# Kernel tuning notes

Hardware: AMD Instinct MI355X
Metric: run time of the kernel (lower is better)

## Reference

```python
import jax, jax.numpy as jnp
from jax import lax
import numpy as np

NPOINT = 1024
RADII = (0.1, 0.2, 0.4)
NSAMPLES = (16, 32, 64)
MLPS = ((64, 64, 128), (128, 128, 256), (128, 128, 256))
IN_CH = 64  # 3 (xyz) + 61 (point features)
EPS = 1e-5


def setup_inputs() -> dict:
    key = jax.random.key(0)
    ks = jax.random.split(key, 64)
    inp = {
        "xyz": jax.random.normal(ks[0], (8, 3, 16384), dtype=jnp.float32),
        "points": jax.random.normal(ks[1], (8, 61, 16384), dtype=jnp.float32),
    }
    ki = 2
    for i, mlp in enumerate(MLPS):
        last = IN_CH
        for j, out_ch in enumerate(mlp):
            inp[f"w{i}{j}"] = jax.random.normal(ks[ki], (out_ch, last), dtype=jnp.float32) * 0.05
            inp[f"b{i}{j}"] = jnp.zeros((out_ch,), dtype=jnp.float32)
            inp[f"g{i}{j}"] = jnp.ones((out_ch,), dtype=jnp.float32)
            inp[f"bt{i}{j}"] = jnp.zeros((out_ch,), dtype=jnp.float32)
            last = out_ch
            ki += 1
    return inp


def square_distance(src, dst):
    # src [B,S,3], dst [B,N,3] -> [B,S,N]
    d = -2.0 * jnp.einsum("bsc,bnc->bsn", src, dst)
    d = d + jnp.sum(src * src, -1)[:, :, None]
    d = d + jnp.sum(dst * dst, -1)[:, None, :]
    return d


def farthest_point_sample(xyz, npoint):
    # xyz [B,N,3] -> idx [B,npoint]; deterministic start at index 0
    B, N, _ = xyz.shape
    def step(carry, _):
        distance, farthest = carry
        centroid = jnp.take_along_axis(xyz, farthest[:, None, None], axis=1)  # [B,1,3]
        dist = jnp.sum((xyz - centroid) ** 2, axis=-1)  # [B,N]
        distance = jnp.minimum(distance, dist)
        return (distance, jnp.argmax(distance, axis=-1).astype(jnp.int32)), farthest
    init = (jnp.full((B, N), 1e10, dtype=xyz.dtype), jnp.zeros((B,), dtype=jnp.int32))
    _, idxs = lax.scan(step, init, None, length=npoint)
    return idxs.T  # [B,npoint]


def gather_points(p, idx):
    # p [B,N,C], idx [B,...] -> [B,...,C]
    B = p.shape[0]
    flat = idx.reshape(B, -1)
    g = jnp.take_along_axis(p, flat[:, :, None], axis=1)
    return g.reshape(idx.shape + (p.shape[-1],))


def query_ball_points(radius, nsample, xyz, new_xyz):
    # xyz [B,N,3], new_xyz [B,S,3] -> idx [B,S,nsample]
    B, N, _ = xyz.shape
    d = square_distance(new_xyz, xyz)  # [B,S,N]
    idx = jnp.broadcast_to(jnp.arange(N, dtype=jnp.int32), d.shape)
    idx = jnp.where(d > radius * radius, N, idx)
    idx = jnp.sort(idx, axis=-1)[:, :, :nsample]
    first = idx[:, :, :1]
    return jnp.where(idx == N, first, idx)


def _forward(xyz, points, params):
    xyz_t = jnp.transpose(xyz, (0, 2, 1))       # [B,N,3]
    pts_t = jnp.transpose(points, (0, 2, 1))    # [B,N,D]
    B, N, _ = xyz_t.shape
    fps_idx = farthest_point_sample(xyz_t, NPOINT)
    new_xyz = gather_points(xyz_t, fps_idx)     # [B,S,3]
    feats = []
    for i, (radius, K) in enumerate(zip(RADII, NSAMPLES)):
        gidx = query_ball_points(radius, K, xyz_t, new_xyz)      # [B,S,K]
        grouped_xyz = gather_points(xyz_t, gidx) - new_xyz[:, :, None, :]
        grouped_pts = gather_points(pts_t, gidx)
        x = jnp.concatenate([grouped_xyz, grouped_pts], axis=-1)  # [B,S,K,IN_CH]
        for (w, b, g, bt) in params[i]:
            x = jnp.einsum("bskc,oc->bsko", x, w) + b  # 1x1 conv
            mean = jnp.mean(x, axis=(0, 1, 2))
            var = jnp.var(x, axis=(0, 1, 2))
            x = jax.nn.relu(g * (x - mean) * lax.rsqrt(var + EPS) + bt)
        feats.append(jnp.max(x, axis=2))  # [B,S,Cout]
    new_points = jnp.transpose(jnp.concatenate(feats, axis=-1), (0, 2, 1))  # [B,640,S]
    return jnp.transpose(new_xyz, (0, 2, 1)), new_points


def reference(xyz, points,
              w00, b00, g00, bt00, w01, b01, g01, bt01, w02, b02, g02, bt02,
              w10, b10, g10, bt10, w11, b11, g11, bt11, w12, b12, g12, bt12,
              w20, b20, g20, bt20, w21, b21, g21, bt21, w22, b22, g22, bt22):
    params = [
        [(w00, b00, g00, bt00), (w01, b01, g01, bt01), (w02, b02, g02, bt02)],
        [(w10, b10, g10, bt10), (w11, b11, g11, bt11), (w12, b12, g12, bt12)],
        [(w20, b20, g20, bt20), (w21, b21, g21, bt21), (w22, b22, g22, bt22)],
    ]
    return _forward(xyz, points, params)
```

## Files before the change

### kernel.cpp

```cpp
#include <hip/hip_runtime.h>
#include <stdint.h>

#define BB 8
#define NN 16384
#define SS 1024

typedef unsigned short u16;
typedef float f32x4 __attribute__((ext_vector_type(4)));
typedef short short8v __attribute__((ext_vector_type(8)));
typedef unsigned short us4 __attribute__((ext_vector_type(4)));
typedef unsigned short us8 __attribute__((ext_vector_type(8)));

static __device__ __forceinline__ float bf2f(u16 u){
    union { uint32_t u; float f; } v; v.u = ((uint32_t)u) << 16; return v.f;
}
static __device__ __forceinline__ u16 f2bf(float f){
    union { float f; uint32_t u; } v; v.f = f;
    return (u16)((v.u + 0x7FFFu + ((v.u >> 16) & 1u)) >> 16);
}
static constexpr int cmax2(int a, int b){ return a > b ? a : b; }

#define LP 12288

__global__ __launch_bounds__(1024) void fps_kernel(const float* __restrict__ xyz,
                                                   float* __restrict__ q,
                                                   float* __restrict__ out_xyz){
#pragma clang fp contract(off)
    __shared__ float lx[LP], ly[LP], lz[LP];
    __shared__ int hist[SS];
    __shared__ unsigned long long slot;
    int b = blockIdx.x;
    int t = threadIdx.x;
    const float* xb = xyz + (size_t)b*3*NN;
    float px[16], py[16], pz[16], dd[16];
#pragma unroll
    for (int j=0;j<16;++j){
        int n = t + j*1024;
        px[j] = xb[n];
        py[j] = xb[NN+n];
        pz[j] = xb[2*NN+n];
        dd[j] = 1e10f;
    }
    for (int idx = t; idx < LP; idx += 1024){
        lx[idx] = xb[idx];
        ly[idx] = xb[NN+idx];
        lz[idx] = xb[2*NN+idx];
    }
    if (t == 0) slot = 0ull;
    __syncthreads();

    int lane = t & 63;
    int far = 0;
    float cx = xb[0], cy = xb[NN], cz = xb[2*NN];
    for (int it=0; it<SS; ++it){
        if (t==0) hist[it] = far;
#pragma unroll
        for (int j=0;j<16;++j){
            asm volatile("" : "+v"(px[j]), "+v"(py[j]), "+v"(pz[j]), "+v"(dd[j]));
        }
#pragma unroll
        for (int j=0;j<16;++j){
            float dx = px[j]-cx, dy = py[j]-cy, dz = pz[j]-cz;
            float d = dx*dx + dy*dy;
            d = d + dz*dz;
            dd[j] = fminf(dd[j], d);
        }
        float m01 = fmaxf(dd[0], dd[1]),  m23 = fmaxf(dd[2], dd[3]);
        float m45 = fmaxf(dd[4], dd[5]),  m67 = fmaxf(dd[6], dd[7]);
        float m89 = fmaxf(dd[8], dd[9]),  mab = fmaxf(dd[10], dd[11]);
        float mcd = fmaxf(dd[12], dd[13]), mef = fmaxf(dd[14], dd[15]);
        float ma = fmaxf(fmaxf(m01, m23), fmaxf(m45, m67));
        float mb = fmaxf(fmaxf(m89, mab), fmaxf(mcd, mef));
        float mx = fmaxf(ma, mb);
        int bj = 0;
#pragma unroll
        for (int j=15; j>=0; --j){
            if (dd[j] == mx) bj = j;
        }
        int bn = t + (bj << 10);
        unsigned long long pk = ((unsigned long long)(unsigned)(it+1) << 46)
                              | ((unsigned long long)__float_as_uint(mx) << 14)
                              | (unsigned long long)(unsigned)(16383 - bn);
#pragma unroll
        for (int off=32; off>0; off>>=1){
            unsigned long long o = __shfl_down(pk, off);
            pk = (o > pk) ? o : pk;
        }
        if (lane == 0) atomicMax(&slot, pk);
        __syncthreads();
        unsigned long long win = slot;
        far = 16383 - (int)(win & 0x3FFFull);
        if (far < LP){
            cx = lx[far]; cy = ly[far]; cz = lz[far];
        } else {
            cx = xb[far]; cy = xb[NN+far]; cz = xb[2*NN+far];
        }
    }
    __syncthreads();
    {
        int s = t;
        int fidx = hist[s];
        float vx, vy, vz;
        if (fidx < LP){ vx = lx[fidx]; vy = ly[fidx]; vz = lz[fidx]; }
        else { vx = xb[fidx]; vy = xb[NN+fidx]; vz = xb[2*NN+fidx]; }
        int gi = b*SS + s;
        q[gi*3+0] = vx; q[gi*3+1] = vy; q[gi*3+2] = vz;
        out_xyz[((size_t)b*3+0)*SS + s] = vx;
        out_xyz[((size_t)b*3+1)*SS + s] = vy;
        out_xyz[((size_t)b*3+2)*SS + s] = vz;
    }
}

__global__ __launch_bounds__(256) void build_ptsT_kernel(const float* __restrict__ xyz, const float* __restrict__ pts,
                                                         float* __restrict__ ptsT){
    __shared__ float tile[64][65];
    int b = blockIdx.y;
    int n0 = blockIdx.x * 64;
    int t = threadIdx.x;
    int ln = t & 63, cr = t >> 6;
    for (int c = cr; c < 64; c += 4){
        float v;
        if (c < 3) v = xyz[((size_t)b*3 + c)*NN + n0 + ln];
        else       v = pts[((size_t)b*61 + (c-3))*NN + n0 + ln];
        tile[ln][c] = v;
    }
    __syncthreads();
    int lc = t & 63, nr = t >> 6;
    for (int n = nr; n < 64; n += 4){
        ptsT[((size_t)b*NN + n0 + n)*64 + lc] = tile[n][lc];
    }
}

__global__ __launch_bounds__(256) void ballquery_kernel(const float* __restrict__ xyz, const float* __restrict__ q,
        int* __restrict__ idx0, int* __restrict__ idx1, int* __restrict__ idx2,
        float r2a, float r2b, float r2c){
#pragma clang fp contract(off)
    __shared__ int lds[4][112];
    int t = threadIdx.x;
    int w = t >> 6, lane = t & 63;
    int qi = blockIdx.x*4 + w;
    int b = qi >> 10;
    const float* xb = xyz + (size_t)b*3*NN;
    float qx = q[qi*3], qy = q[qi*3+1], qz = q[qi*3+2];
    float qn = qx*qx + qy*qy; qn = qn + qz*qz;
    int* l0 = lds[w];
    int* l1 = l0 + 16;
    int* l2 = l0 + 48;
    l0[lane] = 0;
    if (lane < 48) l0[64+lane] = 0;
    int c0=0, c1=0, c2=0;
    uint64_t below = (1ull << lane) - 1ull;
    for (int ch=0; ch<256; ++ch){
        int n = ch*64 + lane;
        float x = xb[n], y = xb[NN+n], z = xb[2*NN+n];
        float dn = x*x + y*y; dn = dn + z*z;
        float dot = qx*x + qy*y; dot = dot + qz*z;
        float d = -2.0f*dot + qn;
        d = d + dn;
        bool o0 = d <= r2a, o1 = d <= r2b, o2 = d <= r2c;
        uint64_t m0 = __ballot(o0), m1 = __ballot(o1), m2 = __ballot(o2);
        if (c0 < 16){
            int p = c0 + (int)__popcll(m0 & below);
            if (o0 && p < 16) l0[p] = n;
            c0 += (int)__popcll(m0); if (c0 > 16) c0 = 16;
        }
        if (c1 < 32){
            int p = c1 + (int)__popcll(m1 & below);
            if (o1 && p < 32) l1[p] = n;
            c1 += (int)__popcll(m1); if (c1 > 32) c1 = 32;
        }
        if (c2 < 64){
            int p = c2 + (int)__popcll(m2 & below);
            if (o2 && p < 64) l2[p] = n;
            c2 += (int)__popcll(m2); if (c2 > 64) c2 = 64;
        }
        if (c0>=16 && c1>=32 && c2>=64) break;
    }
    __syncthreads();
    int f0 = l0[0], f1 = l1[0], f2 = l2[0];
    if (lane >= c0 && lane < 16) l0[lane] = f0;
    if (lane >= c1 && lane < 32) l1[lane] = f1;
    if (lane >= c2)              l2[lane] = f2;
    __syncthreads();
    if (lane < 16) idx0[(size_t)qi*16 + lane] = l0[lane];
    if (lane < 32) idx1[(size_t)qi*32 + lane] = l1[lane];
    idx2[(size_t)qi*64 + lane] = l2[lane];
}

__global__ void convert_w3_kernel(const float* __restrict__ A, int na,
                                  const float* __restrict__ B, int nbb,
                                  const float* __restrict__ C, int nc,
                                  u16* __restrict__ out){
    int i = blockIdx.x*256 + threadIdx.x;
    if (i < na) out[i] = f2bf(A[i]);
    else if (i < na+nbb) out[i] = f2bf(B[i-na]);
    else if (i < na+nbb+nc) out[i] = f2bf(C[i-na-nbb]);
}


template<int CC, int OH>
__device__ __forceinline__ void load_W_frags(const u16* __restrict__ Wb,
                                             short8v (&wf)[CC/32][OH/64],
                                             int l, int w, int hoff){
    int rl = l & 15, kg = l >> 4;
#pragma unroll
    for (int ks=0; ks<CC/32; ++ks)
#pragma unroll
    for (int tc=0; tc<OH/64; ++tc){
        int col = hoff + w*(OH/4) + tc*16 + rl;
        wf[ks][tc] = *(const short8v*)(Wb + (size_t)col*CC + ks*32 + kg*8);
    }
}

template<int K>
__device__ __forceinline__ void stage_A_gather(const float* __restrict__ ptsT, const float* __restrict__ q,
                                               const int* __restrict__ gidx, int m0, int t, char* __restrict__ As){
    int r = t >> 2, q4 = t & 3;
    int m = m0 + r;
    int idx = gidx[m];
    int bs = m / K;
    int b = bs >> 10;
    const float* base = ptsT + ((size_t)b*NN + idx)*64;
    float qx=0.f, qy=0.f, qz=0.f;
    if (q4 == 0){ qx = q[bs*3]; qy = q[bs*3+1]; qz = q[bs*3+2]; }
    int rx = (r & 7) << 4;
#pragma unroll
    for (int ii=0; ii<4; ++ii){
        int c0 = q4*16 + ii*4;
        float4 v = *(const float4*)(base + c0);
        if (q4==0 && ii==0){ v.x -= qx; v.y -= qy; v.z -= qz; }
        us4 u;
        u[0]=f2bf(v.x); u[1]=f2bf(v.y); u[2]=f2bf(v.z); u[3]=f2bf(v.w);
        *(us4*)(As + r*128 + ((c0*2) ^ rx)) = u;
    }
}

template<int OP>
__device__ __forceinline__ void stage_A_z(const u16* __restrict__ zbuf, int m0,
                                          const float* __restrict__ sc, const float* __restrict__ sh,
                                          int t, char* __restrict__ As){
    constexpr int CQ = OP/4;
    for (int s = t; s < 64*CQ; s += 256){
        int r = s / CQ, cq = s - r*CQ;
        us4 zv = *(const us4*)&zbuf[((size_t)(m0+r))*OP + cq*4];
        int c = cq*4;
        us4 u;
        u[0] = f2bf(fmaxf(0.f, bf2f(zv[0])*sc[c+0] + sh[c+0]));
        u[1] = f2bf(fmaxf(0.f, bf2f(zv[1])*sc[c+1] + sh[c+1]));
        u[2] = f2bf(fmaxf(0.f, bf2f(zv[2])*sc[c+2] + sh[c+2]));
        u[3] = f2bf(fmaxf(0.f, bf2f(zv[3])*sc[c+3] + sh[c+3]));
        *(us4*)(As + r*(OP*2) + ((cq*8) ^ ((r&7)<<4))) = u;
    }
}

template<int CC, int OH>
__device__ __forceinline__ void mfma_gemm_v2(const char* __restrict__ As,
                                             const short8v (&wf)[CC/32][OH/64],
                                             f32x4 (&acc)[4][OH/64], int l){
    constexpr int CCB = CC*2;
    int rl = l & 15, kg = l >> 4;
    const char* ap = As + rl*CCB;
    int axor = (rl & 7) << 4;
#pragma unroll
    for (int ks=0; ks<CC/32; ++ks){
        int karg = ((ks<<6) | (kg<<4)) ^ axor;
        short8v a0 = *(const short8v*)(ap + 0*16*CCB + karg);
        short8v a1 = *(const short8v*)(ap + 1*16*CCB + karg);
        short8v a2 = *(const short8v*)(ap + 2*16*CCB + karg);
        short8v a3 = *(const short8v*)(ap + 3*16*CCB + karg);
#pragma unroll
        for (int tc=0; tc<OH/64; ++tc){
            acc[0][tc] = __builtin_amdgcn_mfma_f32_16x16x32_bf16(a0, wf[ks][tc], acc[0][tc], 0,0,0);
            acc[1][tc] = __builtin_amdgcn_mfma_f32_16x16x32_bf16(a1, wf[ks][tc], acc[1][tc], 0,0,0);
            acc[2][tc] = __builtin_amdgcn_mfma_f32_16x16x32_bf16(a2, wf[ks][tc], acc[2][tc], 0,0,0);
            acc[3][tc] = __builtin_amdgcn_mfma_f32_16x16x32_bf16(a3, wf[ks][tc], acc[3][tc], 0,0,0);
        }
    }
}

template<int OH>
__device__ __forceinline__ void bias_mfma(f32x4 (&acc)[4][OH/64], const float* __restrict__ bsrc,
                                          int l, int w, int coff){
#pragma unroll
    for (int tc=0; tc<OH/64; ++tc){
        float bb = bsrc[coff + w*(OH/4) + tc*16 + (l&15)];
#pragma unroll
        for (int tr=0; tr<4; ++tr)
#pragma unroll
        for (int e=0; e<4; ++e) acc[tr][tc][e] += bb;
    }
}

template<int OH, int OT>
__device__ __forceinline__ void zstore_mfma(f32x4 (&acc)[4][OH/64], u16* __restrict__ zbuf,
                                            int m0, int l, int w, int coff){
#pragma unroll
    for (int tr=0; tr<4; ++tr)
#pragma unroll
    for (int e=0; e<4; ++e){
        int row = tr*16 + (l>>4)*4 + e;
#pragma unroll
        for (int tc=0; tc<OH/64; ++tc){
            int c = coff + w*(OH/4) + tc*16 + (l&15);
            zbuf[((size_t)(m0+row))*OT + c] = f2bf(acc[tr][tc][e]);
        }
    }
}

template<int OH, int OT, int K, bool EXT>
__device__ __forceinline__ void stats_mfma(f32x4 (&acc)[4][OH/64], int l, int w, int m0, int blk, int coff,
    float* __restrict__ pS, float* __restrict__ pQ,
    float* __restrict__ gmax, float* __restrict__ gmin){
#pragma unroll
    for (int tc=0; tc<OH/64; ++tc){
        float s1 = 0.f, s2 = 0.f;
        float mxr[4], mnr[4];
#pragma unroll
        for (int tr=0; tr<4; ++tr){
            float v0=acc[tr][tc][0], v1=acc[tr][tc][1], v2=acc[tr][tc][2], v3=acc[tr][tc][3];
            s1 += (v0+v1)+(v2+v3);
            s2 += (v0*v0+v1*v1)+(v2*v2+v3*v3);
            if (EXT){
                mxr[tr] = fmaxf(fmaxf(v0,v1),fmaxf(v2,v3));
                mnr[tr] = fminf(fminf(v0,v1),fminf(v2,v3));
            }
        }
        s1 += __shfl_xor(s1,16); s1 += __shfl_xor(s1,32);
        s2 += __shfl_xor(s2,16); s2 += __shfl_xor(s2,32);
        if (EXT){
#pragma unroll
            for (int tr=0; tr<4; ++tr){
                mxr[tr] = fmaxf(mxr[tr], __shfl_xor(mxr[tr],16));
                mxr[tr] = fmaxf(mxr[tr], __shfl_xor(mxr[tr],32));
                mnr[tr] = fminf(mnr[tr], __shfl_xor(mnr[tr],16));
                mnr[tr] = fminf(mnr[tr], __shfl_xor(mnr[tr],32));
            }
        }
        if (l < 16){
            int c = coff + w*(OH/4) + tc*16 + l;
            pS[(size_t)blk*OT + c] = s1;
            pQ[(size_t)blk*OT + c] = s2;
            if (EXT){
                constexpr int G = 64/K, WG = K/16;
#pragma unroll
                for (int g=0; g<G; ++g){
                    float M1 = mxr[g*WG], M2 = mnr[g*WG];
#pragma unroll
                    for (int ww=1; ww<WG; ++ww){
                        M1 = fmaxf(M1, mxr[g*WG+ww]);
                        M2 = fminf(M2, mnr[g*WG+ww]);
                    }
                    gmax[(size_t)(m0/K + g)*OT + c] = M1;
                    gmin[(size_t)(m0/K + g)*OT + c] = M2;
                }
            }
        }
    }
}

template<int OH>
__device__ __forceinline__ void act_to_As_mfma(f32x4 (&acc)[4][OH/64], const float* __restrict__ bsrc,
    const float* __restrict__ sc, const float* __restrict__ sh, int l, int w, char* __restrict__ As){
#pragma unroll
    for (int tc=0; tc<OH/64; ++tc){
        int c = w*(OH/4) + tc*16 + (l&15);
        float bb = bsrc[c], scv = sc[c], shv = sh[c];
#pragma unroll
        for (int tr=0; tr<4; ++tr)
#pragma unroll
        for (int e=0; e<4; ++e){
            int row = tr*16 + (l>>4)*4 + e;
            float vv = fmaxf(0.f, (acc[tr][tc][e]+bb)*scv + shv);
            *(u16*)(As + row*(OH*2) + ((2*c) ^ ((row&7)<<4))) = f2bf(vv);
        }
    }
}

template<int PHASE, int K, int O1, int O2, int O3>
__global__ __launch_bounds__(256) void fused_mlp(
    const float* __restrict__ ptsT, const float* __restrict__ q, const int* __restrict__ gidx,
    const u16* __restrict__ Wb1, const float* __restrict__ b1,
    const u16* __restrict__ Wb2, const float* __restrict__ b2,
    const u16* __restrict__ Wb3, const float* __restrict__ b3,
    const float* __restrict__ sc1, const float* __restrict__ sh1,
    const float* __restrict__ sc2, const float* __restrict__ sh2,
    float* __restrict__ pS, float* __restrict__ pQ,
    float* __restrict__ gmax, float* __restrict__ gmin,
    u16* __restrict__ zbuf)
{
    constexpr int OH3 = (O3 > 128) ? 128 : O3;
    constexpr int AMX = (PHASE==1) ? 64 : (PHASE==2 ? O1 : (PHASE==3 ? cmax2(O1,O2) : O2));
    __shared__ __align__(16) char As[64*AMX*2];
    int t = threadIdx.x, l = t & 63, w = t >> 6;
    int m0 = blockIdx.x * 64;

    if constexpr (PHASE == 1){
        stage_A_gather<K>(ptsT, q, gidx, m0, t, As);
        short8v wf[2][O1/64];
        load_W_frags<64,O1>(Wb1, wf, l, w, 0);
        __syncthreads();
        f32x4 acc[4][O1/64] = {};
        mfma_gemm_v2<64,O1>(As, wf, acc, l);
        bias_mfma<O1>(acc, b1, l, w, 0);
        if (zbuf) zstore_mfma<O1,O1>(acc, zbuf, m0, l, w, 0);
        stats_mfma<O1,O1,K,false>(acc, l, w, m0, blockIdx.x, 0, pS,pQ,gmax,gmin);
        return;
    }

    if constexpr (PHASE == 2){
        if (zbuf){
            stage_A_z<O1>(zbuf, m0, sc1, sh1, t, As);
        } else {
            stage_A_gather<K>(ptsT, q, gidx, m0, t, As);
            short8v wf1[2][O1/64];
            load_W_frags<64,O1>(Wb1, wf1, l, w, 0);
            __syncthreads();
            f32x4 acc1[4][O1/64] = {};
            mfma_gemm_v2<64,O1>(As, wf1, acc1, l);
            __syncthreads();
            act_to_As_mfma<O1>(acc1, b1, sc1, sh1, l, w, As);
        }
        short8v wf[O1/32][O2/64];
        load_W_frags<O1,O2>(Wb2, wf, l, w, 0);
        __syncthreads();
        f32x4 acc[4][O2/64] = {};
        mfma_gemm_v2<O1,O2>(As, wf, acc, l);
        bias_mfma<O2>(acc, b2, l, w, 0);
        if (zbuf) zstore_mfma<O2,O2>(acc, zbuf, m0, l, w, 0);
        stats_mfma<O2,O2,K,false>(acc, l, w, m0, blockIdx.x, 0, pS,pQ,gmax,gmin);
        return;
    }

    if constexpr (PHASE == 3){
        stage_A_gather<K>(ptsT, q, gidx, m0, t, As);
        short8v wf1[2][O1/64];
        load_W_frags<64,O1>(Wb1, wf1, l, w, 0);
        __syncthreads();
        f32x4 acc1[4][O1/64] = {};
        mfma_gemm_v2<64,O1>(As, wf1, acc1, l);
        __syncthreads();
        act_to_As_mfma<O1>(acc1, b1, sc1, sh1, l, w, As);
        __syncthreads();
        short8v wf2[O1/32][O2/64];
        load_W_frags<O1,O2>(Wb2, wf2, l, w, 0);
        f32x4 acc2[4][O2/64] = {};
        mfma_gemm_v2<O1,O2>(As, wf2, acc2, l);
        __syncthreads();
        act_to_As_mfma<O2>(acc2, b2, sc2, sh2, l, w, As);
    } else {
        stage_A_z<O2>(zbuf, m0, sc2, sh2, t, As);
    }

    __syncthreads();
    constexpr int HH = O3/OH3;
#pragma unroll
    for (int h=0; h<HH; ++h){
        short8v wf[O2/32][OH3/64];
        load_W_frags<O2,OH3>(Wb3, wf, l, w, h*OH3);
        f32x4 acc[4][OH3/64] = {};
        mfma_gemm_v2<O2,OH3>(As, wf, acc, l);
        bias_mfma<OH3>(acc, b3, l, w, h*OH3);
        stats_mfma<OH3,O3,K,true>(acc, l, w, m0, blockIdx.x, h*OH3, pS,pQ,gmax,gmin);
    }
}

__global__ __launch_bounds__(256) void finalize_d_kernel(const float* __restrict__ pS, const float* __restrict__ pQ,
                                      const float* __restrict__ g, const float* __restrict__ bt,
                                      float* __restrict__ sc, float* __restrict__ sh, int nb, double invM){
    __shared__ double red[512];
    int c = blockIdx.x;
    int O = gridDim.x;
    int t = threadIdx.x;
    double S=0.0, Q=0.0;
    for (int v=t; v<nb; v+=256){ S += (double)pS[(size_t)v*O + c]; Q += (double)pQ[(size_t)v*O + c]; }
    red[t]=S; red[256+t]=Q;
    __syncthreads();
    for (int s=128; s>0; s>>=1){
        if (t<s){ red[t]+=red[t+s]; red[256+t]+=red[256+t+s]; }
        __syncthreads();
    }
    if (t==0){
        double mean = red[0]*invM;
        double var  = red[256]*invM - mean*mean;
        double scale = (double)g[c] / sqrt(var + 1e-5);
        sc[c] = (float)scale;
        sh[c] = (float)((double)bt[c] - mean*scale);
    }
}

__global__ void final_out_kernel(const float* __restrict__ gmax, const float* __restrict__ gmin,
                                 const float* __restrict__ sc, const float* __restrict__ sh,
                                 float* __restrict__ outp, int O, int logO, int chbase){
    int gid = blockIdx.x*256 + threadIdx.x;
    int c  = gid & (O-1);
    int bs = gid >> logO;
    int b = bs >> 10, s = bs & 1023;
    float scale = sc[c];
    float v = (scale >= 0.f) ? gmax[gid] : gmin[gid];
    float r = fmaxf(0.f, scale*v + sh[c]);
    outp[((size_t)(b*640 + chbase + c))*SS + s] = r;
}

__global__ void ws_marker_kernel(float* outp, float wsval){ if (threadIdx.x==0) outp[0] = wsval; }

template<int K, int O1, int O2, int O3>
static void run_branch(const float* ptsT, const float* q, const int* gidx,
                       float* pS, float* pQ, float* gmax, float* gmin,
                       float* sc1, float* sh1, float* sc2, float* sh2, float* sc3, float* sh3,
                       u16* z2buf, bool use_z, const u16* wb,
                       void* const* d_in, int wbase, float* np_out, int chbase, hipStream_t stream)
{
    const int M = BB*SS*K;
    const int nb = M/64;
    auto wp = [&](int jl, int which)->const float* { return (const float*)d_in[2 + (wbase+jl)*4 + which]; };
    const double invM = 1.0 / (double)M;
    u16* zb = use_z ? z2buf : (u16*)nullptr;
    const u16* Wb1 = wb;
    const u16* Wb2 = wb + (size_t)O1*64;
    const u16* Wb3 = wb + (size_t)O1*64 + (size_t)O2*O1;

    fused_mlp<1,K,O1,O2,O3><<<nb,256,0,stream>>>(ptsT,q,gidx,
        Wb1,wp(0,1), Wb2,wp(1,1), Wb3,wp(2,1),
        sc1,sh1, sc2,sh2, pS,pQ, gmax,gmin, zb);
    finalize_d_kernel<<<O1,256,0,stream>>>(pS,pQ, wp(0,2), wp(0,3), sc1, sh1, nb, invM);

    fused_mlp<2,K,O1,O2,O3><<<nb,256,0,stream>>>(ptsT,q,gidx,
        Wb1,wp(0,1), Wb2,wp(1,1), Wb3,wp(2,1),
        sc1,sh1, sc2,sh2, pS,pQ, gmax,gmin, zb);
    finalize_d_kernel<<<O2,256,0,stream>>>(pS,pQ, wp(1,2), wp(1,3), sc2, sh2, nb, invM);

    if (use_z){
        fused_mlp<4,K,O1,O2,O3><<<nb,256,0,stream>>>(ptsT,q,gidx,
            Wb1,wp(0,1), Wb2,wp(1,1), Wb3,wp(2,1),
            sc1,sh1, sc2,sh2, pS,pQ, gmax,gmin, z2buf);
    } else {
        fused_mlp<3,K,O1,O2,O3><<<nb,256,0,stream>>>(ptsT,q,gidx,
            Wb1,wp(0,1), Wb2,wp(1,1), Wb3,wp(2,1),
            sc1,sh1, sc2,sh2, pS,pQ, gmax,gmin, nullptr);
    }
    finalize_d_kernel<<<O3,256,0,stream>>>(pS,pQ, wp(2,2), wp(2,3), sc3, sh3, nb, invM);

    final_out_kernel<<<(BB*SS*O3)/256,256,0,stream>>>(gmax,gmin, sc3,sh3, np_out, O3, (O3==256?8:7), chbase);
}

extern "C" void kernel_launch(void* const* d_in, const int* in_sizes, int n_in,
                              void* d_out, int out_size, void* d_ws, size_t ws_size,
                              hipStream_t stream)
{
    const float* xyz = (const float*)d_in[0];
    const float* pts = (const float*)d_in[1];
    float* outp = (float*)d_out;

    char* wsb = (char*)d_ws;
    size_t off = 0;
    auto alloc = [&](size_t bytes) -> void* {
        off = (off + 255) & ~(size_t)255;
        void* p = wsb + off;
        off += bytes;
        return p;
    };
    float* q       = (float*)alloc((size_t)BB*SS*3*4);
    int*   idx0    = (int*)  alloc((size_t)BB*SS*16*4);
    int*   idx1    = (int*)  alloc((size_t)BB*SS*32*4);
    int*   idx2    = (int*)  alloc((size_t)BB*SS*64*4);
    float* ptsT    = (float*)alloc((size_t)BB*NN*64*4);
    float* pS      = (float*)alloc((size_t)8192*256*4);
    float* pQ      = (float*)alloc((size_t)8192*256*4);
    float* gmax    = (float*)alloc((size_t)8192*256*4);
    float* gmin    = (float*)alloc((size_t)8192*256*4);
    float* sc1     = (float*)alloc(256*4);
    float* sh1     = (float*)alloc(256*4);
    float* sc2     = (float*)alloc(256*4);
    float* sh2     = (float*)alloc(256*4);
    float* sc3     = (float*)alloc(256*4);
    float* sh3     = (float*)alloc(256*4);
    u16*   wbf0    = (u16*)  alloc((size_t)16384*2);
    u16*   wbf1    = (u16*)  alloc((size_t)57344*2);
    u16*   wbf2    = (u16*)  alloc((size_t)57344*2);

    if (off > ws_size){
        ws_marker_kernel<<<1,64,0,stream>>>(outp, (float)ws_size);
        return;
    }

    u16* z2buf = (u16*)alloc((size_t)BB*SS*64*128*2);
    bool use_z = (off <= ws_size);

    auto wptr = [&](int layer)->const float* { return (const float*)d_in[2 + layer*4 + 0]; };
    convert_w3_kernel<<<64, 256, 0, stream>>>(wptr(0), 4096, wptr(1), 4096, wptr(2), 8192, wbf0);
    convert_w3_kernel<<<224, 256, 0, stream>>>(wptr(3), 8192, wptr(4), 16384, wptr(5), 32768, wbf1);
    convert_w3_kernel<<<224, 256, 0, stream>>>(wptr(6), 8192, wptr(7), 16384, wptr(8), 32768, wbf2);

    build_ptsT_kernel<<<dim3(NN/64, BB), 256, 0, stream>>>(xyz, pts, ptsT);
    fps_kernel<<<BB, 1024, 0, stream>>>(xyz, q, outp);

    const float r2a = (float)(0.1*0.1);
    const float r2b = (float)(0.2*0.2);
    const float r2c = (float)(0.4*0.4);
    ballquery_kernel<<<2048, 256, 0, stream>>>(xyz, q, idx0, idx1, idx2, r2a, r2b, r2c);

    float* np_out = outp + (size_t)BB*3*SS;
    run_branch<16, 64, 64,128>(ptsT, q, idx0, pS,pQ, gmax,gmin, sc1,sh1,sc2,sh2,sc3,sh3, z2buf, use_z, wbf0, d_in, 0, np_out,   0, stream);
    run_branch<32,128,128,256>(ptsT, q, idx1, pS,pQ, gmax,gmin, sc1,sh1,sc2,sh2,sc3,sh3, z2buf, use_z, wbf1, d_in, 3, np_out, 128, stream);
    run_branch<64,128,128,256>(ptsT, q, idx2, pS,pQ, gmax,gmin, sc1,sh1,sc2,sh2,sc3,sh3, z2buf, use_z, wbf2, d_in, 6, np_out, 384, stream);

    hipError_t e = hipGetLastError();
    if (e != hipSuccess){
        ws_marker_kernel<<<1,64,0,stream>>>(outp, 1000.0f + (float)(int)e);
    }
}
```

Before: 2.853 ms.

## Fuse FPS, point transpose and weight conversion into one heterogeneous kernel

Merges the FPS kernel, the point-feature transpose kernel and the three weight-conversion kernels into one launch. Block ranges select the role: the first 8 blocks run FPS and the rest do the transpose and bf16 conversion, so the memory-bound prep work runs alongside the serial FPS loop. It also moves the asm register barrier out of the FPS iteration loop. In exchange, the transpose and conversion blocks now use 1024 threads and the large FPS shared-memory footprint, which may limit how many of them fit per CU.

```diff
diff --git a/kernel.cpp b/kernel.cpp
--- a/kernel.cpp
+++ b/kernel.cpp
@@ -21,16 +21,61 @@
 static constexpr int cmax2(int a, int b){ return a > b ? a : b; }
 
 #define LP 12288
-
-__global__ __launch_bounds__(1024) void fps_kernel(const float* __restrict__ xyz,
-                                                   float* __restrict__ q,
-                                                   float* __restrict__ out_xyz){
+#define SM_FPS (LP*3*4 + SS*4 + 8)
+
+__global__ __launch_bounds__(1024) void pre_kernel(
+        const float* __restrict__ xyz, const float* __restrict__ pts,
+        float* __restrict__ ptsT, float* __restrict__ q, float* __restrict__ out_xyz,
+        const float* __restrict__ w0, const float* __restrict__ w1, const float* __restrict__ w2,
+        const float* __restrict__ w3, const float* __restrict__ w4, const float* __restrict__ w5,
+        const float* __restrict__ w6, const float* __restrict__ w7, const float* __restrict__ w8,
+        u16* __restrict__ wbf0, u16* __restrict__ wbf1, u16* __restrict__ wbf2){
 #pragma clang fp contract(off)
-    __shared__ float lx[LP], ly[LP], lz[LP];
-    __shared__ int hist[SS];
-    __shared__ unsigned long long slot;
+    __shared__ __align__(16) char smem_raw[SM_FPS];
+    int t = threadIdx.x;
+
+    if (blockIdx.x >= 8){
+        int bx = blockIdx.x - 8;
+        if (bx < 2048){
+            float (*tile)[65] = (float (*)[65])smem_raw;
+            int b = bx >> 8;
+            int n0 = (bx & 255) * 64;
+            int ln = t & 63, cr = t >> 6;
+            for (int c = cr; c < 64; c += 16){
+                float v;
+                if (c < 3) v = xyz[((size_t)b*3 + c)*NN + n0 + ln];
+                else       v = pts[((size_t)b*61 + (c-3))*NN + n0 + ln];
+                tile[ln][c] = v;
+            }
+            __syncthreads();
+            int lc = t & 63, nr = t >> 6;
+            for (int n = nr; n < 64; n += 16){
+                ptsT[((size_t)b*NN + n0 + n)*64 + lc] = tile[n][lc];
+            }
+        } else {
+            int br = bx - 2048;
+            const float* A; const float* B; const float* C; u16* out; int na, nb2, nc;
+            if (br == 0){ A=w0; na=4096;  B=w1; nb2=4096;  C=w2; nc=8192;  out=wbf0; }
+            else if (br == 1){ A=w3; na=8192; B=w4; nb2=16384; C=w5; nc=32768; out=wbf1; }
+            else { A=w6; na=8192; B=w7; nb2=16384; C=w8; nc=32768; out=wbf2; }
+            int tot = na + nb2 + nc;
+            for (int i = t; i < tot; i += 1024){
+                float v;
+                if (i < na) v = A[i];
+                else if (i < na+nb2) v = B[i-na];
+                else v = C[i-na-nb2];
+                out[i] = f2bf(v);
+            }
+        }
+        return;
+    }
+
+    float* lx = (float*)smem_raw;
+    float* ly = lx + LP;
+    float* lz = ly + LP;
+    int*  hist = (int*)(lz + LP);
+    unsigned long long* slotp = (unsigned long long*)(hist + SS);
     int b = blockIdx.x;
-    int t = threadIdx.x;
     const float* xb = xyz + (size_t)b*3*NN;
     float px[16], py[16], pz[16], dd[16];
 #pragma unroll
@@ -41,12 +86,16 @@
         pz[j] = xb[2*NN+n];
         dd[j] = 1e10f;
     }
+#pragma unroll
+    for (int j=0;j<16;++j){
+        asm volatile("" : "+v"(px[j]), "+v"(py[j]), "+v"(pz[j]));
+    }
     for (int idx = t; idx < LP; idx += 1024){
         lx[idx] = xb[idx];
         ly[idx] = xb[NN+idx];
         lz[idx] = xb[2*NN+idx];
     }
-    if (t == 0) slot = 0ull;
+    if (t == 0) *slotp = 0ull;
     __syncthreads();
 
     int lane = t & 63;
@@ -54,10 +103,6 @@
     float cx = xb[0], cy = xb[NN], cz = xb[2*NN];
     for (int it=0; it<SS; ++it){
         if (t==0) hist[it] = far;
-#pragma unroll
-        for (int j=0;j<16;++j){
-            asm volatile("" : "+v"(px[j]), "+v"(py[j]), "+v"(pz[j]), "+v"(dd[j]));
-        }
 #pragma unroll
         for (int j=0;j<16;++j){
             float dx = px[j]-cx, dy = py[j]-cy, dz = pz[j]-cz;
@@ -86,9 +131,9 @@
             unsigned long long o = __shfl_down(pk, off);
             pk = (o > pk) ? o : pk;
         }
-        if (lane == 0) atomicMax(&slot, pk);
-        __syncthreads();
-        unsigned long long win = slot;
+        if (lane == 0) atomicMax(slotp, pk);
+        __syncthreads();
+        unsigned long long win = *slotp;
         far = 16383 - (int)(win & 0x3FFFull);
         if (far < LP){
             cx = lx[far]; cy = ly[far]; cz = lz[far];
@@ -108,26 +153,6 @@
         out_xyz[((size_t)b*3+0)*SS + s] = vx;
         out_xyz[((size_t)b*3+1)*SS + s] = vy;
         out_xyz[((size_t)b*3+2)*SS + s] = vz;
-    }
-}
-
-__global__ __launch_bounds__(256) void build_ptsT_kernel(const float* __restrict__ xyz, const float* __restrict__ pts,
-                                                         float* __restrict__ ptsT){
-    __shared__ float tile[64][65];
-    int b = blockIdx.y;
-    int n0 = blockIdx.x * 64;
-    int t = threadIdx.x;
-    int ln = t & 63, cr = t >> 6;
-    for (int c = cr; c < 64; c += 4){
-        float v;
-        if (c < 3) v = xyz[((size_t)b*3 + c)*NN + n0 + ln];
-        else       v = pts[((size_t)b*61 + (c-3))*NN + n0 + ln];
-        tile[ln][c] = v;
-    }
-    __syncthreads();
-    int lc = t & 63, nr = t >> 6;
-    for (int n = nr; n < 64; n += 4){
-        ptsT[((size_t)b*NN + n0 + n)*64 + lc] = tile[n][lc];
     }
 }
 
@@ -187,16 +212,6 @@
     idx2[(size_t)qi*64 + lane] = l2[lane];
 }
 
-__global__ void convert_w3_kernel(const float* __restrict__ A, int na,
-                                  const float* __restrict__ B, int nbb,
-                                  const float* __restrict__ C, int nc,
-                                  u16* __restrict__ out){
-    int i = blockIdx.x*256 + threadIdx.x;
-    if (i < na) out[i] = f2bf(A[i]);
-    else if (i < na+nbb) out[i] = f2bf(B[i-na]);
-    else if (i < na+nbb+nc) out[i] = f2bf(C[i-na-nbb]);
-}
-
 
 template<int CC, int OH>
 __device__ __forceinline__ void load_W_frags(const u16* __restrict__ Wb,
@@ -587,12 +602,11 @@
     bool use_z = (off <= ws_size);
 
     auto wptr = [&](int layer)->const float* { return (const float*)d_in[2 + layer*4 + 0]; };
-    convert_w3_kernel<<<64, 256, 0, stream>>>(wptr(0), 4096, wptr(1), 4096, wptr(2), 8192, wbf0);
-    convert_w3_kernel<<<224, 256, 0, stream>>>(wptr(3), 8192, wptr(4), 16384, wptr(5), 32768, wbf1);
-    convert_w3_kernel<<<224, 256, 0, stream>>>(wptr(6), 8192, wptr(7), 16384, wptr(8), 32768, wbf2);
-
-    build_ptsT_kernel<<<dim3(NN/64, BB), 256, 0, stream>>>(xyz, pts, ptsT);
-    fps_kernel<<<BB, 1024, 0, stream>>>(xyz, q, outp);
+
+    pre_kernel<<<8 + 2048 + 3, 1024, 0, stream>>>(
+        xyz, pts, ptsT, q, outp,
+        wptr(0), wptr(1), wptr(2), wptr(3), wptr(4), wptr(5), wptr(6), wptr(7), wptr(8),
+        wbf0, wbf1, wbf2);
 
     const float r2a = (float)(0.1*0.1);
     const float r2b = (float)(0.2*0.2);
```

New measurement: 2.756 ms (median of 3 runs). 1.04x faster.
